# Kernel tuning notes

Measured on AMD Instinct MI355X. Metric: run time of the kernel, lower is better.

## Reference

```python
import jax, jax.numpy as jnp
import numpy as np

N_NODES = 100000
N_EDGES = 6400000


def setup_inputs() -> dict:
    key = jax.random.key(0)
    k1, k2, k3, k4, k5, k6 = jax.random.split(key, 6)
    edge_predictions = jax.random.normal(k1, (N_EDGES,), dtype=jnp.float32)
    node_predictions = jax.random.normal(k2, (N_NODES,), dtype=jnp.float32)
    x = jax.random.uniform(k3, (N_NODES, 4), dtype=jnp.float32)  # col 2 = demand
    capacity = jnp.ones((1,), dtype=jnp.float32) * 50.0  # vehicle capacity
    y_edges = (jax.random.uniform(k4, (N_EDGES,)) < 0.1).astype(jnp.float32)
    y_nodes = jax.random.normal(k5, (N_NODES,), dtype=jnp.float32)
    edge_index = jax.random.randint(k6, (2, N_EDGES), 0, N_NODES, dtype=jnp.int64)
    return {
        'edge_predictions': edge_predictions,
        'node_predictions': node_predictions,
        'x': x,
        'capacity': capacity,
        'y_edges': y_edges,
        'y_nodes': y_nodes,
        'edge_index': edge_index,
        'num_nodes': N_NODES,
    }


def _bce_with_logits(logits, targets):
    # numerically stable elementwise BCE-with-logits
    return jnp.maximum(logits, 0.0) - logits * targets + jnp.log1p(jnp.exp(-jnp.abs(logits)))


def _focal_loss(logits, targets, alpha=0.25, gamma=2.0):
    bce = _bce_with_logits(logits, targets)
    probs = jax.nn.sigmoid(logits)
    p_t = probs * targets + (1.0 - probs) * (1.0 - targets)
    alpha_t = alpha * targets + (1.0 - alpha) * (1.0 - targets)
    return jnp.mean(alpha_t * (1.0 - p_t) ** gamma * bce)


def reference(edge_predictions, node_predictions, x, capacity, y_edges, y_nodes,
              edge_index, num_nodes):
    edge_probs = jax.nn.sigmoid(edge_predictions)
    src, dst = edge_index[0], edge_index[1]

    # single segment-sum pass over edges replaces the O(num_nodes * num_edges) loops
    in_sums = jax.ops.segment_sum(edge_probs, dst, num_segments=num_nodes)   # [N]
    out_sums = jax.ops.segment_sum(edge_probs, src, num_segments=num_nodes)  # [N]

    # coverage loss: customer nodes (1..N-1) should have in/out degree-prob == 1
    coverage = (jnp.sum((in_sums[1:] - 1.0) ** 2) + jnp.sum((out_sums[1:] - 1.0) ** 2)) \
               / (2.0 * max(num_nodes - 1, 1))

    # tour formation: flow conservation over ALL nodes
    tour_formation = jnp.sum((in_sums - out_sums) ** 2) / num_nodes

    # depot balance
    depot_balance = (in_sums[0] - out_sums[0]) ** 2

    # capacity tours: depot out-degree ~ ceil(total_demand / capacity)
    demands = x[:, 2]
    total_demand = jnp.sum(demands[1:])
    cap_value = jax.lax.stop_gradient(jnp.mean(capacity))  # torch uses .item()
    expected_tours = jnp.ceil(total_demand / cap_value)
    capacity_tours = (out_sums[0] - expected_tours) ** 2

    # similarity (focal) loss on raw logits
    similarity = _focal_loss(edge_predictions, y_edges, alpha=0.25, gamma=2.0)

    # masked node MSE (mask is data-dependent -> where-based mean)
    mask = (y_nodes >= 0.0).astype(node_predictions.dtype)
    cnt = jnp.maximum(jnp.sum(mask), 1.0)
    node_loss = jnp.sum(mask * (node_predictions - y_nodes) ** 2) / cnt

    total = (coverage * 5.0 + tour_formation * 3.0 + depot_balance * 2.0 +
             capacity_tours * 1.5 + similarity * 0.3 + node_loss * 0.1)
    return total
```

## Files before the change

### kernel.cpp

```cpp
#include <hip/hip_runtime.h>
#include <math.h>

#define RANGE_LOG 9
#define RANGE 512
#define NBUCK_MAX 256
#define CAP 70000u
#define EDGES_PER_CHUNK 4096
#define SCAT_THREADS 512
#define EPT 8
#define PARTS 8



__device__ __forceinline__ float wave_reduce_sum(float v) {
    #pragma unroll
    for (int o = 32; o > 0; o >>= 1) v += __shfl_down(v, o, 64);
    return v;
}

template <int NW>
__device__ float block_reduce_sum(float v) {
    __shared__ float s[NW];
    __syncthreads();
    const int lane = threadIdx.x & 63;
    const int wid  = threadIdx.x >> 6;
    v = wave_reduce_sum(v);
    if (lane == 0) s[wid] = v;
    __syncthreads();
    float r = 0.f;
    if (wid == 0) {
        float x = (lane < NW) ? s[lane] : 0.f;
        r = wave_reduce_sum(x);
    }
    return r;
}

#define LOG2E 1.44269504f
#define LN2   0.69314718f

__device__ __forceinline__ float fast_focal(float x, float t, float& p) {
    const float ax = fabsf(x);
    const float e  = __builtin_amdgcn_exp2f(-ax * LOG2E);
    const float r  = __builtin_amdgcn_rcpf(1.f + e);
    p = (x >= 0.f) ? r : 1.f - r;
    const float sp  = __builtin_amdgcn_logf(1.f + e) * LN2;
    const float bce = fmaxf(x, 0.f) - x * t + sp;
    const float p_t = p * t + (1.f - p) * (1.f - t);
    const float a_t = 0.25f * t + 0.75f * (1.f - t);
    const float om  = 1.f - p_t;
    return a_t * om * om * bce;
}


__global__ __launch_bounds__(SCAT_THREADS, 8)
void scatter_kernel(const float* __restrict__ ep,
                    const float* __restrict__ ye,
                    const int*   __restrict__ ei,
                    unsigned* __restrict__ cursor,
                    unsigned* __restrict__ pairs,
                    float* __restrict__ acc,
                    int E) {
    __shared__ unsigned s_hist[NBUCK_MAX];
    __shared__ unsigned s_cur[NBUCK_MAX];
    __shared__ unsigned s_off[NBUCK_MAX];
    __shared__ unsigned s_gbase[NBUCK_MAX];
    __shared__ unsigned s_pack[2 * EDGES_PER_CHUNK];

    const int tid   = threadIdx.x;
    const int ebase = blockIdx.x * EDGES_PER_CHUNK;
    const int ec    = min(EDGES_PER_CHUNK, E - ebase);
    const int cnt   = 2 * ec;

    if (tid < NBUCK_MAX) s_hist[tid] = 0u;
    __syncthreads();

    unsigned pk[2 * EPT];
    float local = 0.f;
    const int  le0  = tid * EPT;
    const bool full = (le0 + EPT) <= ec;

    if (full) {
        const int e0 = ebase + le0;
        #pragma unroll
        for (int h = 0; h < 2; ++h) {
            const float4 xv = *(const float4*)(ep + e0 + 4 * h);
            const float4 tv = *(const float4*)(ye + e0 + 4 * h);
            const int4   sv = *(const int4*)(ei + e0 + 4 * h);
            const int4   dv = *(const int4*)(ei + E + e0 + 4 * h);
            const float xx[4] = {xv.x, xv.y, xv.z, xv.w};
            const float tt[4] = {tv.x, tv.y, tv.z, tv.w};
            const unsigned ss[4] = {(unsigned)sv.x, (unsigned)sv.y, (unsigned)sv.z, (unsigned)sv.w};
            const unsigned dd[4] = {(unsigned)dv.x, (unsigned)dv.y, (unsigned)dv.z, (unsigned)dv.w};
            #pragma unroll
            for (int j = 0; j < 4; ++j) {
                float p;
                local += fast_focal(xx[j], tt[j], p);
                const unsigned pq = min((unsigned)(p * 16384.f + 0.5f), 16383u);
                const int k = 4 * h + j;
                pk[2 * k]     = (ss[j] << 15) | pq;
                pk[2 * k + 1] = (dd[j] << 15) | 16384u | pq;
                atomicAdd(&s_hist[ss[j] >> RANGE_LOG], 1u);
                atomicAdd(&s_hist[dd[j] >> RANGE_LOG], 1u);
            }
        }
    } else {
        #pragma unroll
        for (int k = 0; k < EPT; ++k) {
            pk[2 * k] = 0xFFFFFFFFu;
            pk[2 * k + 1] = 0xFFFFFFFFu;
            const int el = le0 + k;
            if (el < ec) {
                const int e = ebase + el;
                float p;
                local += fast_focal(ep[e], ye[e], p);
                const unsigned pq = min((unsigned)(p * 16384.f + 0.5f), 16383u);
                const unsigned s = (unsigned)ei[e];
                const unsigned d = (unsigned)ei[E + e];
                pk[2 * k]     = (s << 15) | pq;
                pk[2 * k + 1] = (d << 15) | 16384u | pq;
                atomicAdd(&s_hist[s >> RANGE_LOG], 1u);
                atomicAdd(&s_hist[d >> RANGE_LOG], 1u);
            }
        }
    }
    __syncthreads();

    if (tid < NBUCK_MAX) s_cur[tid] = s_hist[tid];
    __syncthreads();
    for (int d = 1; d < NBUCK_MAX; d <<= 1) {
        unsigned v = 0u;
        if (tid < NBUCK_MAX) {
            v = s_cur[tid];
            if (tid >= d) v += s_cur[tid - d];
        }
        __syncthreads();
        if (tid < NBUCK_MAX) s_cur[tid] = v;
        __syncthreads();
    }
    if (tid < NBUCK_MAX) {
        const unsigned c    = s_hist[tid];
        const unsigned excl = s_cur[tid] - c;
        s_off[tid]   = excl;
        s_cur[tid]   = excl;
        s_gbase[tid] = c ? atomicAdd(&cursor[tid], c) : 0u;
    }
    __syncthreads();

    if (full) {
        #pragma unroll
        for (int k = 0; k < 2 * EPT; ++k) {
            const unsigned v = pk[k];
            const unsigned r = atomicAdd(&s_cur[v >> 24], 1u);
            s_pack[r] = v;
        }
    } else {
        #pragma unroll
        for (int k = 0; k < 2 * EPT; ++k) {
            const unsigned v = pk[k];
            if (v != 0xFFFFFFFFu) {
                const unsigned r = atomicAdd(&s_cur[v >> 24], 1u);
                s_pack[r] = v;
            }
        }
    }
    __syncthreads();

    for (int idx = tid; idx < cnt; idx += SCAT_THREADS) {
        const unsigned v = s_pack[idx];
        const unsigned b = v >> 24;
        pairs[(size_t)b * CAP + s_gbase[b] + ((unsigned)idx - s_off[b])] = v;
    }

    const float bs = block_reduce_sum<SCAT_THREADS / 64>(local);
    if (tid == 0) atomicAdd(&acc[0], bs);
}

__global__ __launch_bounds__(256, 8)
void accum_kernel(const unsigned* __restrict__ cursor,
                  const unsigned* __restrict__ pairs,
                  unsigned* __restrict__ partials,
                  int N, int nbuck) {
    __shared__ unsigned sAcc[2 * RANGE];
    const int tid  = threadIdx.x;
    const int b    = blockIdx.x % nbuck;
    const int part = blockIdx.x / nbuck;
    for (int i = tid; i < 2 * RANGE; i += 256) sAcc[i] = 0u;
    __syncthreads();

    unsigned fill = cursor[b];
    if (fill > CAP) fill = CAP;
    const unsigned lo = ((unsigned)(((unsigned long long)fill * part) / PARTS)) & ~3u;
    const unsigned hi = (part == PARTS - 1)
        ? fill
        : (((unsigned)(((unsigned long long)fill * (part + 1)) / PARTS)) & ~3u);
    const size_t gb = (size_t)b * CAP;
    const unsigned hiv = lo + ((hi - lo) & ~3u);

    for (unsigned i = lo + 4 * tid; i < hiv; i += 4 * 256) {
        const uint4 v = *(const uint4*)(pairs + gb + i);
        atomicAdd(&sAcc[(v.x >> 14) & 1023u], v.x & 16383u);
        atomicAdd(&sAcc[(v.y >> 14) & 1023u], v.y & 16383u);
        atomicAdd(&sAcc[(v.z >> 14) & 1023u], v.z & 16383u);
        atomicAdd(&sAcc[(v.w >> 14) & 1023u], v.w & 16383u);
    }
    for (unsigned i = hiv + tid; i < hi; i += 256) {
        const unsigned v = pairs[gb + i];
        atomicAdd(&sAcc[(v >> 14) & 1023u], v & 16383u);
    }
    __syncthreads();

    const int nodes = min(RANGE, N - b * RANGE);
    unsigned* dstp = partials + (size_t)part * 2 * N + 2 * (size_t)(b * RANGE);
    for (int i = tid; i < nodes; i += 256) {
        *(uint2*)(dstp + 2 * i) = *(const uint2*)(&sAcc[2 * i]);
    }
}

__global__ void node_cov2_kernel(const float* __restrict__ npred,
                                 const float* __restrict__ yn,
                                 const float* __restrict__ x,
                                 const unsigned* __restrict__ partials,
                                 float* __restrict__ acc,
                                 int N) {
    const int i = blockIdx.x * blockDim.x + threadIdx.x;
    float dem = 0.f, cntm = 0.f, sq = 0.f, cov = 0.f, tour = 0.f;
    if (i < N) {
        unsigned ou = 0u, iu = 0u;
        #pragma unroll
        for (int p = 0; p < PARTS; ++p) {
            const uint2 v = *(const uint2*)(partials + (size_t)p * 2 * N + 2 * (size_t)i);
            ou += v.x;
            iu += v.y;
        }
        const float outv = (float)ou * (1.f / 16384.f);
        const float inv  = (float)iu * (1.f / 16384.f);
        if (i >= 1) dem = x[i * 4 + 2];
        const float y = yn[i];
        if (y >= 0.f) {
            cntm = 1.f;
            const float d = npred[i] - y;
            sq = d * d;
        }
        const float dd = inv - outv;
        tour = dd * dd;
        if (i >= 1) cov = (inv - 1.f) * (inv - 1.f) + (outv - 1.f) * (outv - 1.f);
        if (i == 0) { acc[6] = inv; acc[7] = outv; }
    }
    float r;
    r = block_reduce_sum<4>(dem);  if (threadIdx.x == 0) atomicAdd(&acc[1], r);
    r = block_reduce_sum<4>(cntm); if (threadIdx.x == 0) atomicAdd(&acc[2], r);
    r = block_reduce_sum<4>(sq);   if (threadIdx.x == 0) atomicAdd(&acc[3], r);
    r = block_reduce_sum<4>(cov);  if (threadIdx.x == 0) atomicAdd(&acc[4], r);
    r = block_reduce_sum<4>(tour); if (threadIdx.x == 0) atomicAdd(&acc[5], r);
}

__global__ void final2_kernel(const float* __restrict__ acc,
                              const float* __restrict__ capacity,
                              float* __restrict__ out,
                              int N, int E) {
    const float coverage = acc[4] / (2.0f * (float)(N - 1));
    const float tour     = acc[5] / (float)N;
    const float in0  = acc[6];
    const float out0 = acc[7];
    const float depot = (in0 - out0) * (in0 - out0);
    const float cap = capacity[0];
    const float expected = ceilf(acc[1] / cap);
    const float cap_t = (out0 - expected) * (out0 - expected);
    const float sim = acc[0] / (float)E;
    const float node_loss = acc[3] / fmaxf(acc[2], 1.f);
    out[0] = coverage * 5.f + tour * 3.f + depot * 2.f + cap_t * 1.5f +
             sim * 0.3f + node_loss * 0.1f;
}


__global__ void edge_kernel(const float* __restrict__ ep,
                            const float* __restrict__ ye,
                            const int*   __restrict__ src,
                            const int*   __restrict__ dst,
                            float* __restrict__ in_sums,
                            float* __restrict__ out_sums,
                            float* __restrict__ acc,
                            int E) {
    float local = 0.f;
    for (int i = blockIdx.x * blockDim.x + threadIdx.x; i < E;
         i += gridDim.x * blockDim.x) {
        const float x = ep[i];
        float p;
        local += fast_focal(x, ye[i], p);
        unsafeAtomicAdd(&out_sums[src[i]], p);
        unsafeAtomicAdd(&in_sums[dst[i]], p);
    }
    const float bs = block_reduce_sum<4>(local);
    if (threadIdx.x == 0) atomicAdd(&acc[0], bs);
}

__global__ void node_cov_kernel(const float* __restrict__ npred,
                                const float* __restrict__ yn,
                                const float* __restrict__ x,
                                const float* __restrict__ in_sums,
                                const float* __restrict__ out_sums,
                                float* __restrict__ acc,
                                int N) {
    const int i = blockIdx.x * blockDim.x + threadIdx.x;
    float dem = 0.f, cntm = 0.f, sq = 0.f, cov = 0.f, tour = 0.f;
    if (i < N) {
        if (i >= 1) dem = x[i * 4 + 2];
        const float y = yn[i];
        if (y >= 0.f) {
            cntm = 1.f;
            const float d = npred[i] - y;
            sq = d * d;
        }
        const float a = in_sums[i];
        const float b = out_sums[i];
        const float dd = a - b;
        tour = dd * dd;
        if (i >= 1) cov = (a - 1.f) * (a - 1.f) + (b - 1.f) * (b - 1.f);
        if (i == 0) { acc[6] = a; acc[7] = b; }
    }
    float r;
    r = block_reduce_sum<4>(dem);  if (threadIdx.x == 0) atomicAdd(&acc[1], r);
    r = block_reduce_sum<4>(cntm); if (threadIdx.x == 0) atomicAdd(&acc[2], r);
    r = block_reduce_sum<4>(sq);   if (threadIdx.x == 0) atomicAdd(&acc[3], r);
    r = block_reduce_sum<4>(cov);  if (threadIdx.x == 0) atomicAdd(&acc[4], r);
    r = block_reduce_sum<4>(tour); if (threadIdx.x == 0) atomicAdd(&acc[5], r);
}


extern "C" void kernel_launch(void* const* d_in, const int* in_sizes, int n_in,
                              void* d_out, int out_size, void* d_ws, size_t ws_size,
                              hipStream_t stream) {
    const float* ep       = (const float*)d_in[0];
    const float* npred    = (const float*)d_in[1];
    const float* x        = (const float*)d_in[2];
    const float* capacity = (const float*)d_in[3];
    const float* ye       = (const float*)d_in[4];
    const float* yn       = (const float*)d_in[5];
    const int*   ei       = (const int*)d_in[6];

    const int E = in_sizes[0];
    const int N = in_sizes[1];
    const int nbuck = (N + RANGE - 1) / RANGE;

    char* w = (char*)d_ws;
    float*    acc      = (float*)w;
    unsigned* cursor   = (unsigned*)(w + 256);
    unsigned* partials = (unsigned*)(w + 4096);
    size_t off_pairs = 4096 + (size_t)PARTS * 2 * N * sizeof(unsigned);
    off_pairs = (off_pairs + 255) & ~(size_t)255;
    unsigned* pairs = (unsigned*)(w + off_pairs);
    const size_t need = off_pairs + (size_t)nbuck * CAP * sizeof(unsigned) + 65536;

    if (nbuck <= NBUCK_MAX && ws_size >= need && (E % 4) == 0) {
        hipMemsetAsync(d_ws, 0, 4096, stream);
        const int nchunks = (E + EDGES_PER_CHUNK - 1) / EDGES_PER_CHUNK;
        scatter_kernel<<<nchunks, SCAT_THREADS, 0, stream>>>(
            ep, ye, ei, cursor, pairs, acc, E);
        accum_kernel<<<nbuck * PARTS, 256, 0, stream>>>(
            cursor, pairs, partials, N, nbuck);
        node_cov2_kernel<<<(N + 255) / 256, 256, 0, stream>>>(
            npred, yn, x, partials, acc, N);
        final2_kernel<<<1, 1, 0, stream>>>(acc, capacity, (float*)d_out, N, E);
    } else {
        float* in_sums  = (float*)(w + 4096);
        float* out_sums = in_sums + N;
        hipMemsetAsync(d_ws, 0, 4096 + (size_t)2 * N * sizeof(float), stream);
        edge_kernel<<<4096, 256, 0, stream>>>(ep, ye, ei, ei + E, in_sums,
                                              out_sums, acc, E);
        node_cov_kernel<<<(N + 255) / 256, 256, 0, stream>>>(
            npred, yn, x, in_sums, out_sums, acc, N);
        final2_kernel<<<1, 1, 0, stream>>>(acc, capacity, (float*)d_out, N, E);
    }
}
```

Baseline: 198.5 us.

## Pack edge records into 16-bit entries with narrower buckets and fuse final reduction

The bucketed edge records shrink from 32-bit to 16-bit. Buckets now span 256 nodes, and each record holds an 8-bit local node id, a direction bit and a 7-bit quantized probability. This roughly halves the global write and read traffic of the intermediate pair buffer between the scatter and accumulate kernels. The per-block bucket prefix scan now uses wave shuffles instead of a barrier-heavy loop, and the final single-thread kernel is folded into the last block of the node kernel through an atomic counter. In exchange, edge-probability precision drops from 14 to 7 bits, which adds quantization error to the in/out degree sums.

```diff
diff --git a/kernel.cpp b/kernel.cpp
--- a/kernel.cpp
+++ b/kernel.cpp
@@ -1,14 +1,14 @@
 #include <hip/hip_runtime.h>
 #include <math.h>
 
-#define RANGE_LOG 9
-#define RANGE 512
-#define NBUCK_MAX 256
-#define CAP 70000u
+#define RANGE_LOG 8
+#define RANGE 256
+#define NB_META 512
+#define CAP 34400u
 #define EDGES_PER_CHUNK 4096
 #define SCAT_THREADS 512
 #define EPT 8
-#define PARTS 8
+#define PARTS 4
 
 
 
@@ -57,21 +57,22 @@
                     const float* __restrict__ ye,
                     const int*   __restrict__ ei,
                     unsigned* __restrict__ cursor,
-                    unsigned* __restrict__ pairs,
+                    unsigned short* __restrict__ pairs,
                     float* __restrict__ acc,
                     int E) {
-    __shared__ unsigned s_hist[NBUCK_MAX];
-    __shared__ unsigned s_cur[NBUCK_MAX];
-    __shared__ unsigned s_off[NBUCK_MAX];
-    __shared__ unsigned s_gbase[NBUCK_MAX];
+    __shared__ unsigned s_hist[NB_META];
+    __shared__ unsigned s_cur[NB_META];
+    __shared__ unsigned s_gbase[NB_META];
     __shared__ unsigned s_pack[2 * EDGES_PER_CHUNK];
 
     const int tid   = threadIdx.x;
+    const int lane  = tid & 63;
+    const int wid   = tid >> 6;
     const int ebase = blockIdx.x * EDGES_PER_CHUNK;
     const int ec    = min(EDGES_PER_CHUNK, E - ebase);
     const int cnt   = 2 * ec;
 
-    if (tid < NBUCK_MAX) s_hist[tid] = 0u;
+    s_hist[tid] = 0u;
     __syncthreads();
 
     unsigned pk[2 * EPT];
@@ -95,12 +96,13 @@
             for (int j = 0; j < 4; ++j) {
                 float p;
                 local += fast_focal(xx[j], tt[j], p);
-                const unsigned pq = min((unsigned)(p * 16384.f + 0.5f), 16383u);
+                const unsigned pq = min((unsigned)(p * 128.f + 0.5f), 127u);
                 const int k = 4 * h + j;
-                pk[2 * k]     = (ss[j] << 15) | pq;
-                pk[2 * k + 1] = (dd[j] << 15) | 16384u | pq;
-                atomicAdd(&s_hist[ss[j] >> RANGE_LOG], 1u);
-                atomicAdd(&s_hist[dd[j] >> RANGE_LOG], 1u);
+                const unsigned sb = ss[j] >> RANGE_LOG, db = dd[j] >> RANGE_LOG;
+                pk[2 * k]     = (sb << 16) | ((ss[j] & (RANGE - 1)) << 8) | pq;
+                pk[2 * k + 1] = (db << 16) | ((dd[j] & (RANGE - 1)) << 8) | 128u | pq;
+                atomicAdd(&s_hist[sb], 1u);
+                atomicAdd(&s_hist[db], 1u);
             }
         }
     } else {
@@ -113,62 +115,69 @@
                 const int e = ebase + el;
                 float p;
                 local += fast_focal(ep[e], ye[e], p);
-                const unsigned pq = min((unsigned)(p * 16384.f + 0.5f), 16383u);
+                const unsigned pq = min((unsigned)(p * 128.f + 0.5f), 127u);
                 const unsigned s = (unsigned)ei[e];
                 const unsigned d = (unsigned)ei[E + e];
-                pk[2 * k]     = (s << 15) | pq;
-                pk[2 * k + 1] = (d << 15) | 16384u | pq;
-                atomicAdd(&s_hist[s >> RANGE_LOG], 1u);
-                atomicAdd(&s_hist[d >> RANGE_LOG], 1u);
+                const unsigned sb = s >> RANGE_LOG, db = d >> RANGE_LOG;
+                pk[2 * k]     = (sb << 16) | ((s & (RANGE - 1)) << 8) | pq;
+                pk[2 * k + 1] = (db << 16) | ((d & (RANGE - 1)) << 8) | 128u | pq;
+                atomicAdd(&s_hist[sb], 1u);
+                atomicAdd(&s_hist[db], 1u);
             }
         }
     }
     __syncthreads();
 
-    if (tid < NBUCK_MAX) s_cur[tid] = s_hist[tid];
-    __syncthreads();
-    for (int d = 1; d < NBUCK_MAX; d <<= 1) {
-        unsigned v = 0u;
-        if (tid < NBUCK_MAX) {
-            v = s_cur[tid];
-            if (tid >= d) v += s_cur[tid - d];
-        }
-        __syncthreads();
-        if (tid < NBUCK_MAX) s_cur[tid] = v;
-        __syncthreads();
-    }
-    if (tid < NBUCK_MAX) {
-        const unsigned c    = s_hist[tid];
-        const unsigned excl = s_cur[tid] - c;
-        s_off[tid]   = excl;
-        s_cur[tid]   = excl;
-        s_gbase[tid] = c ? atomicAdd(&cursor[tid], c) : 0u;
-    }
+    const unsigned h = s_hist[tid];
+    unsigned v = h;
+    #pragma unroll
+    for (int o = 1; o < 64; o <<= 1) {
+        const unsigned t = (unsigned)__shfl_up((int)v, o, 64);
+        if (lane >= o) v += t;
+    }
+    if (lane == 63) s_gbase[wid] = v;
+    __syncthreads();
+    if (wid == 0 && lane < 8) {
+        unsigned x = s_gbase[lane];
+        #pragma unroll
+        for (int o = 1; o < 8; o <<= 1) {
+            const unsigned t = (unsigned)__shfl_up((int)x, o, 8);
+            if (lane >= o) x += t;
+        }
+        s_gbase[lane] = x;
+    }
+    __syncthreads();
+    const unsigned wbase = (wid > 0) ? s_gbase[wid - 1] : 0u;
+    __syncthreads();
+    const unsigned excl = wbase + v - h;
+    s_cur[tid]   = excl;
+    s_gbase[tid] = h ? (atomicAdd(&cursor[tid], h) - excl) : 0u;
     __syncthreads();
 
     if (full) {
         #pragma unroll
         for (int k = 0; k < 2 * EPT; ++k) {
-            const unsigned v = pk[k];
-            const unsigned r = atomicAdd(&s_cur[v >> 24], 1u);
-            s_pack[r] = v;
+            const unsigned pv = pk[k];
+            const unsigned r = atomicAdd(&s_cur[pv >> 16], 1u);
+            s_pack[r] = pv;
         }
     } else {
         #pragma unroll
         for (int k = 0; k < 2 * EPT; ++k) {
-            const unsigned v = pk[k];
-            if (v != 0xFFFFFFFFu) {
-                const unsigned r = atomicAdd(&s_cur[v >> 24], 1u);
-                s_pack[r] = v;
+            const unsigned pv = pk[k];
+            if (pv != 0xFFFFFFFFu) {
+                const unsigned r = atomicAdd(&s_cur[pv >> 16], 1u);
+                s_pack[r] = pv;
             }
         }
     }
     __syncthreads();
 
     for (int idx = tid; idx < cnt; idx += SCAT_THREADS) {
-        const unsigned v = s_pack[idx];
-        const unsigned b = v >> 24;
-        pairs[(size_t)b * CAP + s_gbase[b] + ((unsigned)idx - s_off[b])] = v;
+        const unsigned pv = s_pack[idx];
+        const unsigned b  = pv >> 16;
+        pairs[(size_t)b * CAP + (unsigned)(s_gbase[b] + (unsigned)idx)] =
+            (unsigned short)pv;
     }
 
     const float bs = block_reduce_sum<SCAT_THREADS / 64>(local);
@@ -177,35 +186,40 @@
 
 __global__ __launch_bounds__(256, 8)
 void accum_kernel(const unsigned* __restrict__ cursor,
-                  const unsigned* __restrict__ pairs,
+                  const unsigned short* __restrict__ pairs,
                   unsigned* __restrict__ partials,
                   int N, int nbuck) {
     __shared__ unsigned sAcc[2 * RANGE];
     const int tid  = threadIdx.x;
     const int b    = blockIdx.x % nbuck;
     const int part = blockIdx.x / nbuck;
-    for (int i = tid; i < 2 * RANGE; i += 256) sAcc[i] = 0u;
+    sAcc[tid] = 0u; sAcc[tid + 256] = 0u;
     __syncthreads();
 
     unsigned fill = cursor[b];
     if (fill > CAP) fill = CAP;
-    const unsigned lo = ((unsigned)(((unsigned long long)fill * part) / PARTS)) & ~3u;
+    const unsigned lo = ((unsigned)(((unsigned long long)fill * part) / PARTS)) & ~7u;
     const unsigned hi = (part == PARTS - 1)
         ? fill
-        : (((unsigned)(((unsigned long long)fill * (part + 1)) / PARTS)) & ~3u);
+        : (((unsigned)(((unsigned long long)fill * (part + 1)) / PARTS)) & ~7u);
     const size_t gb = (size_t)b * CAP;
-    const unsigned hiv = lo + ((hi - lo) & ~3u);
-
-    for (unsigned i = lo + 4 * tid; i < hiv; i += 4 * 256) {
+    const unsigned hiv = lo + ((hi - lo) & ~7u);
+
+    for (unsigned i = lo + 8 * tid; i < hiv; i += 8 * 256) {
         const uint4 v = *(const uint4*)(pairs + gb + i);
-        atomicAdd(&sAcc[(v.x >> 14) & 1023u], v.x & 16383u);
-        atomicAdd(&sAcc[(v.y >> 14) & 1023u], v.y & 16383u);
-        atomicAdd(&sAcc[(v.z >> 14) & 1023u], v.z & 16383u);
-        atomicAdd(&sAcc[(v.w >> 14) & 1023u], v.w & 16383u);
+        const unsigned d0 = v.x, d1 = v.y, d2 = v.z, d3 = v.w;
+        atomicAdd(&sAcc[(d0 & 0xFFFFu) >> 7], d0 & 127u);
+        atomicAdd(&sAcc[(d0 >> 23)], (d0 >> 16) & 127u);
+        atomicAdd(&sAcc[(d1 & 0xFFFFu) >> 7], d1 & 127u);
+        atomicAdd(&sAcc[(d1 >> 23)], (d1 >> 16) & 127u);
+        atomicAdd(&sAcc[(d2 & 0xFFFFu) >> 7], d2 & 127u);
+        atomicAdd(&sAcc[(d2 >> 23)], (d2 >> 16) & 127u);
+        atomicAdd(&sAcc[(d3 & 0xFFFFu) >> 7], d3 & 127u);
+        atomicAdd(&sAcc[(d3 >> 23)], (d3 >> 16) & 127u);
     }
     for (unsigned i = hiv + tid; i < hi; i += 256) {
-        const unsigned v = pairs[gb + i];
-        atomicAdd(&sAcc[(v >> 14) & 1023u], v & 16383u);
+        const unsigned u = pairs[gb + i];
+        atomicAdd(&sAcc[u >> 7], u & 127u);
     }
     __syncthreads();
 
@@ -216,12 +230,16 @@
     }
 }
 
-__global__ void node_cov2_kernel(const float* __restrict__ npred,
+__global__ void node_cov3_kernel(const float* __restrict__ npred,
                                  const float* __restrict__ yn,
                                  const float* __restrict__ x,
                                  const unsigned* __restrict__ partials,
                                  float* __restrict__ acc,
-                                 int N) {
+                                 const float* __restrict__ capacity,
+                                 float* __restrict__ out,
+                                 unsigned* __restrict__ done,
+                                 int N, int E) {
+    __shared__ bool is_last;
     const int i = blockIdx.x * blockDim.x + threadIdx.x;
     float dem = 0.f, cntm = 0.f, sq = 0.f, cov = 0.f, tour = 0.f;
     if (i < N) {
@@ -232,8 +250,8 @@
             ou += v.x;
             iu += v.y;
         }
-        const float outv = (float)ou * (1.f / 16384.f);
-        const float inv  = (float)iu * (1.f / 16384.f);
+        const float outv = (float)ou * (1.f / 128.f);
+        const float inv  = (float)iu * (1.f / 128.f);
         if (i >= 1) dem = x[i * 4 + 2];
         const float y = yn[i];
         if (y >= 0.f) {
@@ -244,7 +262,7 @@
         const float dd = inv - outv;
         tour = dd * dd;
         if (i >= 1) cov = (inv - 1.f) * (inv - 1.f) + (outv - 1.f) * (outv - 1.f);
-        if (i == 0) { acc[6] = inv; acc[7] = outv; }
+        if (i == 0) { atomicAdd(&acc[6], inv); atomicAdd(&acc[7], outv); }
     }
     float r;
     r = block_reduce_sum<4>(dem);  if (threadIdx.x == 0) atomicAdd(&acc[1], r);
@@ -252,24 +270,28 @@
     r = block_reduce_sum<4>(sq);   if (threadIdx.x == 0) atomicAdd(&acc[3], r);
     r = block_reduce_sum<4>(cov);  if (threadIdx.x == 0) atomicAdd(&acc[4], r);
     r = block_reduce_sum<4>(tour); if (threadIdx.x == 0) atomicAdd(&acc[5], r);
-}
-
-__global__ void final2_kernel(const float* __restrict__ acc,
-                              const float* __restrict__ capacity,
-                              float* __restrict__ out,
-                              int N, int E) {
-    const float coverage = acc[4] / (2.0f * (float)(N - 1));
-    const float tour     = acc[5] / (float)N;
-    const float in0  = acc[6];
-    const float out0 = acc[7];
-    const float depot = (in0 - out0) * (in0 - out0);
-    const float cap = capacity[0];
-    const float expected = ceilf(acc[1] / cap);
-    const float cap_t = (out0 - expected) * (out0 - expected);
-    const float sim = acc[0] / (float)E;
-    const float node_loss = acc[3] / fmaxf(acc[2], 1.f);
-    out[0] = coverage * 5.f + tour * 3.f + depot * 2.f + cap_t * 1.5f +
-             sim * 0.3f + node_loss * 0.1f;
+
+    if (threadIdx.x == 0) {
+        __threadfence();
+        const unsigned t = atomicAdd(done, 1u);
+        is_last = (t == (unsigned)(gridDim.x - 1));
+    }
+    __syncthreads();
+    if (is_last && threadIdx.x == 0) {
+        __threadfence();
+        const float coverage = acc[4] / (2.0f * (float)(N - 1));
+        const float tourv    = acc[5] / (float)N;
+        const float in0  = acc[6];
+        const float out0 = acc[7];
+        const float depot = (in0 - out0) * (in0 - out0);
+        const float cap = capacity[0];
+        const float expected = ceilf(acc[1] / cap);
+        const float cap_t = (out0 - expected) * (out0 - expected);
+        const float sim = acc[0] / (float)E;
+        const float node_loss = acc[3] / fmaxf(acc[2], 1.f);
+        out[0] = coverage * 5.f + tourv * 3.f + depot * 2.f + cap_t * 1.5f +
+                 sim * 0.3f + node_loss * 0.1f;
+    }
 }
 
 
@@ -300,7 +322,11 @@
                                 const float* __restrict__ in_sums,
                                 const float* __restrict__ out_sums,
                                 float* __restrict__ acc,
-                                int N) {
+                                const float* __restrict__ capacity,
+                                float* __restrict__ out,
+                                unsigned* __restrict__ done,
+                                int N, int E) {
+    __shared__ bool is_last;
     const int i = blockIdx.x * blockDim.x + threadIdx.x;
     float dem = 0.f, cntm = 0.f, sq = 0.f, cov = 0.f, tour = 0.f;
     if (i < N) {
@@ -316,7 +342,7 @@
         const float dd = a - b;
         tour = dd * dd;
         if (i >= 1) cov = (a - 1.f) * (a - 1.f) + (b - 1.f) * (b - 1.f);
-        if (i == 0) { acc[6] = a; acc[7] = b; }
+        if (i == 0) { atomicAdd(&acc[6], a); atomicAdd(&acc[7], b); }
     }
     float r;
     r = block_reduce_sum<4>(dem);  if (threadIdx.x == 0) atomicAdd(&acc[1], r);
@@ -324,6 +350,25 @@
     r = block_reduce_sum<4>(sq);   if (threadIdx.x == 0) atomicAdd(&acc[3], r);
     r = block_reduce_sum<4>(cov);  if (threadIdx.x == 0) atomicAdd(&acc[4], r);
     r = block_reduce_sum<4>(tour); if (threadIdx.x == 0) atomicAdd(&acc[5], r);
+
+    if (threadIdx.x == 0) {
+        __threadfence();
+        const unsigned t = atomicAdd(done, 1u);
+        is_last = (t == (unsigned)(gridDim.x - 1));
+    }
+    __syncthreads();
+    if (is_last && threadIdx.x == 0) {
+        __threadfence();
+        const float coverage = acc[4] / (2.0f * (float)(N - 1));
+        const float tourv    = acc[5] / (float)N;
+        const float depot = (acc[6] - acc[7]) * (acc[6] - acc[7]);
+        const float expected = ceilf(acc[1] / capacity[0]);
+        const float cap_t = (acc[7] - expected) * (acc[7] - expected);
+        const float sim = acc[0] / (float)E;
+        const float node_loss = acc[3] / fmaxf(acc[2], 1.f);
+        out[0] = coverage * 5.f + tourv * 3.f + depot * 2.f + cap_t * 1.5f +
+                 sim * 0.3f + node_loss * 0.1f;
+    }
 }
 
 
@@ -343,24 +388,24 @@
     const int nbuck = (N + RANGE - 1) / RANGE;
 
     char* w = (char*)d_ws;
-    float*    acc      = (float*)w;
-    unsigned* cursor   = (unsigned*)(w + 256);
+    float*    acc    = (float*)w;
+    unsigned* cursor = (unsigned*)(w + 256);
+    unsigned* done   = (unsigned*)(w + 3840);
     unsigned* partials = (unsigned*)(w + 4096);
     size_t off_pairs = 4096 + (size_t)PARTS * 2 * N * sizeof(unsigned);
     off_pairs = (off_pairs + 255) & ~(size_t)255;
-    unsigned* pairs = (unsigned*)(w + off_pairs);
-    const size_t need = off_pairs + (size_t)nbuck * CAP * sizeof(unsigned) + 65536;
-
-    if (nbuck <= NBUCK_MAX && ws_size >= need && (E % 4) == 0) {
+    unsigned short* pairs = (unsigned short*)(w + off_pairs);
+    const size_t need = off_pairs + (size_t)nbuck * CAP * sizeof(unsigned short) + 65536;
+
+    if (nbuck <= NB_META && ws_size >= need && (E % 4) == 0 && N < (1 << 17)) {
         hipMemsetAsync(d_ws, 0, 4096, stream);
         const int nchunks = (E + EDGES_PER_CHUNK - 1) / EDGES_PER_CHUNK;
         scatter_kernel<<<nchunks, SCAT_THREADS, 0, stream>>>(
             ep, ye, ei, cursor, pairs, acc, E);
         accum_kernel<<<nbuck * PARTS, 256, 0, stream>>>(
             cursor, pairs, partials, N, nbuck);
-        node_cov2_kernel<<<(N + 255) / 256, 256, 0, stream>>>(
-            npred, yn, x, partials, acc, N);
-        final2_kernel<<<1, 1, 0, stream>>>(acc, capacity, (float*)d_out, N, E);
+        node_cov3_kernel<<<(N + 255) / 256, 256, 0, stream>>>(
+            npred, yn, x, partials, acc, capacity, (float*)d_out, done, N, E);
     } else {
         float* in_sums  = (float*)(w + 4096);
         float* out_sums = in_sums + N;
@@ -368,7 +413,7 @@
         edge_kernel<<<4096, 256, 0, stream>>>(ep, ye, ei, ei + E, in_sums,
                                               out_sums, acc, E);
         node_cov_kernel<<<(N + 255) / 256, 256, 0, stream>>>(
-            npred, yn, x, in_sums, out_sums, acc, N);
-        final2_kernel<<<1, 1, 0, stream>>>(acc, capacity, (float*)d_out, N, E);
-    }
-}
+            npred, yn, x, in_sums, out_sums, acc, capacity, (float*)d_out,
+            done, N, E);
+    }
+}
```

Result: no change. 194.9 us (-1.8%).
